# Optimization experiments

Hardware: AMD Instinct MI355X
Metric: run time of the kernel (lower is better)

The kernel has to match this reference:

```python
import jax, jax.numpy as jnp
import numpy as np
import math

B, N, H, TDIM, K, R = 32, 4096, 256, 128, 2, 2


def setup_inputs() -> dict:
    key = jax.random.key(0)
    ks = jax.random.split(key, 12)
    s = 1.0 / math.sqrt(H)
    gain = 1.414
    return {
        "x": jax.random.normal(ks[0], (B, N), jnp.float32),
        "t": jax.random.uniform(ks[1], (B,), jnp.float32),
        # scaled so repeated L@x stays O(1) over Chebyshev hops
        "laplacian": jax.random.normal(ks[2], (N, N), jnp.float32) / math.sqrt(N),
        "w_g1": jax.random.normal(ks[3], (1, H, K + 1), jnp.float32) * gain / math.sqrt(1 + H),
        "w_g2": jax.random.normal(ks[4], (H, 1, K + 1), jnp.float32) * gain / math.sqrt(1 + H),
        "w_t1": jax.random.normal(ks[5], (TDIM, H), jnp.float32) / math.sqrt(TDIM),
        "b_t1": jnp.zeros((H,), jnp.float32),
        "w_t2": jax.random.normal(ks[6], (H, H), jnp.float32) * s,
        "b_t2": jnp.zeros((H,), jnp.float32),
        "w_map": jax.random.normal(ks[7], (N, H), jnp.float32) / math.sqrt(N),
        "b_map": jnp.zeros((H,), jnp.float32),
        "res_w": jax.random.normal(ks[8], (R, 3, H, H), jnp.float32) * s,
        "res_b": jnp.zeros((R, 3, H), jnp.float32),
        "w_o1": jax.random.normal(ks[9], (H, H), jnp.float32) * s,
        "b_o1": jnp.zeros((H,), jnp.float32),
        "w_o2": jax.random.normal(ks[10], (H, N), jnp.float32) * s,
        "b_o2": jnp.zeros((N,), jnp.float32),
    }


def timestep_embedding(t, dim, max_period=10000):
    half = dim // 2  # dim is even here
    freqs = jnp.exp(-math.log(max_period) * jnp.arange(half, dtype=t.dtype) / half)
    args = t[:, None] * freqs[None, :]  # [B, half]
    return jnp.concatenate([jnp.cos(args), jnp.sin(args)], axis=-1)  # [B, dim]


def gcn_layer(L, x, w, conv_order):
    xs = [x]
    h = x
    for _ in range(conv_order):
        h = jnp.einsum('mn,bnc->bmc', L, h)  # sparse-style Laplacian propagation (dense here)
        xs.append(h)
    X = jnp.stack(xs, axis=-1)  # [B, N, C, K+1]
    return jnp.einsum('bnik,iok->bno', X, w)


def reference(x, t, laplacian, w_g1, w_g2, w_t1, b_t1, w_t2, b_t2,
              w_map, b_map, res_w, res_b, w_o1, b_o1, w_o2, b_o2):
    silu = jax.nn.silu
    # time embedding path: sinusoidal -> Linear -> SiLU -> Linear
    temb = timestep_embedding(t, TDIM)
    t_out = silu(temb @ w_t1 + b_t1) @ w_t2 + b_t2  # [B, H]
    # GCNBlock: two Chebyshev GCN layers (GCNLayer.forward applies no activation)
    g = gcn_layer(laplacian, x[:, :, None], w_g1, K)  # [B, N, H]
    g = gcn_layer(laplacian, g, w_g2, K)[..., 0]      # [B, N]
    # ResNet_FC on the node signal
    h = g @ w_map + b_map  # [B, H]
    inv_sqrt2 = 1.0 / math.sqrt(2.0)
    for r in range(R):
        z = h
        for i in range(3):
            z = silu(z @ res_w[r, i] + res_b[r, i])
        h = (h + z) * inv_sqrt2
    # output head with time conditioning
    out = silu((h + t_out) @ w_o1 + b_o1) @ w_o2 + b_o2  # [B, N]
    return out
```

## Files before the change

### kernel.cpp

```cpp
#include <hip/hip_runtime.h>
#include <hip/hip_bf16.h>

typedef __bf16 bf16x8 __attribute__((ext_vector_type(8)));
typedef __bf16 bf16x4 __attribute__((ext_vector_type(4)));
typedef float  f32x4  __attribute__((ext_vector_type(4)));


static constexpr size_t WS_A     = 0;
static constexpr size_t WS_TOUT  = 1024;
static constexpr size_t WS_H0    = 65536;
static constexpr size_t WS_UB    = 131072;
static constexpr size_t WS_XB    = 262144;
static constexpr size_t WS_G2B   = 524288;
static constexpr size_t WS_ZB    = 1048576;
static constexpr size_t WS_ZF    = 2097152;
static constexpr size_t WS_WMAPT = 4194304;
static constexpr size_t WS_WO2T  = 6291456;
static constexpr size_t WS_LB    = 8388608;

__device__ __forceinline__ f32x4 mfma16(bf16x8 a, bf16x8 b, f32x4 c) {
    return __builtin_amdgcn_mfma_f32_16x16x32_bf16(a, b, c, 0, 0, 0);
}

__device__ __forceinline__ bf16x8 cvt8(const float* p) {
    f32x4 lo = *(const f32x4*)p;
    f32x4 hi = *(const f32x4*)(p + 4);
    bf16x8 r;
    r[0] = (__bf16)lo[0]; r[1] = (__bf16)lo[1]; r[2] = (__bf16)lo[2]; r[3] = (__bf16)lo[3];
    r[4] = (__bf16)hi[0]; r[5] = (__bf16)hi[1]; r[6] = (__bf16)hi[2]; r[7] = (__bf16)hi[3];
    return r;
}

__device__ __forceinline__ float silu_f(float x) { return x / (1.0f + __expf(-x)); }

__device__ __forceinline__ void transpose_tile(const float* __restrict__ src, int sstride,
                                               __bf16* __restrict__ dst, int dstride,
                                               int r0, int c0, float* sh, int tid) {
    const int r = tid >> 3, cg = (tid & 7) * 4;
    f32x4 v = *(const f32x4*)(src + (size_t)(r0 + r) * sstride + c0 + cg);
    sh[r * 33 + cg + 0] = v[0];
    sh[r * 33 + cg + 1] = v[1];
    sh[r * 33 + cg + 2] = v[2];
    sh[r * 33 + cg + 3] = v[3];
    __syncthreads();
    bf16x4 o;
    o[0] = (__bf16)sh[(cg + 0) * 33 + r];
    o[1] = (__bf16)sh[(cg + 1) * 33 + r];
    o[2] = (__bf16)sh[(cg + 2) * 33 + r];
    o[3] = (__bf16)sh[(cg + 3) * 33 + r];
    *(bf16x4*)(dst + (size_t)(c0 + r) * dstride + r0 + cg) = o;
}

__global__ __launch_bounds__(256) void prep_kernel(
    const float* __restrict__ x, const float* __restrict__ t,
    const float* __restrict__ w_g1, const float* __restrict__ w_g2,
    const float* __restrict__ w_t1, const float* __restrict__ b_t1,
    const float* __restrict__ w_t2, const float* __restrict__ b_t2,
    const float* __restrict__ w_map, const float* __restrict__ w_o2,
    char* __restrict__ ws)
{
    __shared__ float sh[1056];
    const int bi = blockIdx.x, tid = threadIdx.x;
    if (bi == 0) {
        const float g10 = w_g1[tid * 3 + 0], g11 = w_g1[tid * 3 + 1], g12 = w_g1[tid * 3 + 2];
        const float g20 = w_g2[tid * 3 + 0], g21 = w_g2[tid * 3 + 1], g22 = w_g2[tid * 3 + 2];
        float p[9] = {g10 * g20, g10 * g21, g10 * g22,
                      g11 * g20, g11 * g21, g11 * g22,
                      g12 * g20, g12 * g21, g12 * g22};
        const int wv = tid >> 6, ln = tid & 63;
#pragma unroll
        for (int j = 0; j < 9; ++j) {
            float v = p[j];
#pragma unroll
            for (int off = 32; off > 0; off >>= 1) v += __shfl_down(v, off);
            if (ln == 0) sh[wv * 9 + j] = v;
        }
        __syncthreads();
        if (tid == 0) {
            float s[9];
#pragma unroll
            for (int j = 0; j < 9; ++j) s[j] = sh[j] + sh[9 + j] + sh[18 + j] + sh[27 + j];
            float* a = (float*)(ws + WS_A);
            a[0] = s[0];
            a[1] = s[1] + s[3];
            a[2] = s[2] + s[4] + s[6];
            a[3] = s[5] + s[7];
            a[4] = s[8];
        }
    } else if (bi < 33) {
        const int b = bi - 1;
        float* t_out = (float*)(ws + WS_TOUT);
        if (tid < 64) {
            float fr = __expf(-9.210340371976184f * (float)tid * (1.0f / 64.0f));
            float ang = t[b] * fr;
            sh[tid]      = __cosf(ang);
            sh[64 + tid] = __sinf(ang);
        }
        __syncthreads();
        float acc = b_t1[tid];
        for (int j = 0; j < 128; ++j) acc += sh[j] * w_t1[j * 256 + tid];
        sh[128 + tid] = silu_f(acc);
        __syncthreads();
        float acc2 = b_t2[tid];
        for (int j = 0; j < 256; ++j) acc2 += sh[128 + j] * w_t2[j * 256 + tid];
        t_out[b * 256 + tid] = acc2;
    } else if (bi < 35) {
        f32x4* p = (f32x4*)(ws + WS_H0);
        f32x4 z = {0.f, 0.f, 0.f, 0.f};
        p[(bi - 33) * 256 + tid] = z;
    } else if (bi < 99) {
        const int e = ((bi - 35) * 256 + tid) * 8;
        *(bf16x8*)((__bf16*)(ws + WS_XB) + e) = cvt8(x + e);
    } else if (bi < 1123) {
        const int ti = bi - 99;
        transpose_tile(w_map, 256, (__bf16*)(ws + WS_WMAPT), 4096,
                       (ti >> 3) * 32, (ti & 7) * 32, sh, tid);
    } else {
        const int ti = bi - 1123;
        transpose_tile(w_o2, 4096, (__bf16*)(ws + WS_WO2T), 256,
                       (ti & 7) * 32, (ti >> 3) * 32, sh, tid);
    }
}

__global__ __launch_bounds__(1024) void hop1_kernel(
    const float* __restrict__ L, const __bf16* __restrict__ xb,
    float* __restrict__ zf_out, __bf16* __restrict__ zb_out,
    __bf16* __restrict__ Lb)
{
    __shared__ float red[16][16][33];
    const int bi = blockIdx.x, tid = threadIdx.x;
    const int wave = tid >> 6, lane = tid & 63;
    const int l15 = lane & 15, q = lane >> 4;
    const int m0 = bi * 16;
    const int kbase = wave * 256;

    const float*  lp  = L  + (size_t)(m0 + l15) * 4096;
    __bf16*       lbp = Lb + (size_t)(m0 + l15) * 4096;
    const __bf16* b0p = xb + (size_t)l15 * 4096;
    const __bf16* b1p = xb + (size_t)(l15 + 16) * 4096;

    f32x4 acc0 = {0,0,0,0}, acc1 = {0,0,0,0};
#pragma unroll
    for (int ks = 0; ks < 8; ++ks) {
        const int k = kbase + ks * 32 + q * 8;
        bf16x8 a  = cvt8(lp + k);
        *(bf16x8*)(lbp + k) = a;
        bf16x8 b0 = *(const bf16x8*)(b0p + k);
        bf16x8 b1 = *(const bf16x8*)(b1p + k);
        acc0 = mfma16(a, b0, acc0);
        acc1 = mfma16(a, b1, acc1);
    }
#pragma unroll
    for (int r = 0; r < 4; ++r) {
        red[wave][q * 4 + r][l15]      = acc0[r];
        red[wave][q * 4 + r][l15 + 16] = acc1[r];
    }
    __syncthreads();
    if (tid < 512) {
        const int m = tid & 15, b = tid >> 4;
        float v = 0.f;
#pragma unroll
        for (int w = 0; w < 16; ++w) v += red[w][m][b];
        zf_out[(size_t)b * 4096 + m0 + m] = v;
        zb_out[(size_t)b * 4096 + m0 + m] = (__bf16)v;
    }
}

__global__ __launch_bounds__(1024) void hop_mid_split(
    const __bf16* __restrict__ Lb, const __bf16* __restrict__ zb_in,
    float* __restrict__ zf_out, __bf16* __restrict__ zb_out)
{
    __shared__ float red[16][16][17];
    const int bi = blockIdx.x, tid = threadIdx.x;
    const int wave = tid >> 6, lane = tid & 63;
    const int l15 = lane & 15, q = lane >> 4;
    const int bg = bi & 1;
    const int m0 = (bi >> 1) * 16;
    const int kbase = wave * 256;

    const __bf16* ap  = Lb + (size_t)(m0 + l15) * 4096;
    const __bf16* b0p = zb_in + (size_t)(bg * 16 + l15) * 4096;

    f32x4 acc0 = {0,0,0,0};
#pragma unroll
    for (int ks = 0; ks < 8; ++ks) {
        const int k = kbase + ks * 32 + q * 8;
        bf16x8 a  = *(const bf16x8*)(ap + k);
        bf16x8 b0 = *(const bf16x8*)(b0p + k);
        acc0 = mfma16(a, b0, acc0);
    }
#pragma unroll
    for (int r = 0; r < 4; ++r)
        red[wave][q * 4 + r][l15] = acc0[r];
    __syncthreads();
    if (tid < 256) {
        const int m = tid & 15, b = tid >> 4;
        float v = 0.f;
#pragma unroll
        for (int w = 0; w < 16; ++w) v += red[w][m][b];
        const size_t idx = (size_t)(bg * 16 + b) * 4096 + m0 + m;
        zf_out[idx] = v;
        zb_out[idx] = (__bf16)v;
    }
}

__global__ __launch_bounds__(1024) void hop4_split(
    const __bf16* __restrict__ Lb, const __bf16* __restrict__ zb_in,
    const float* __restrict__ x,
    const float* __restrict__ z1f, const float* __restrict__ z2f,
    const float* __restrict__ z3f, const float* __restrict__ a_c,
    __bf16* __restrict__ g2b)
{
    __shared__ float red[16][16][17];
    const int bi = blockIdx.x, tid = threadIdx.x;
    const int wave = tid >> 6, lane = tid & 63;
    const int l15 = lane & 15, q = lane >> 4;
    const int bg = bi & 1;
    const int m0 = (bi >> 1) * 16;
    const int kbase = wave * 256;

    const __bf16* ap  = Lb + (size_t)(m0 + l15) * 4096;
    const __bf16* b0p = zb_in + (size_t)(bg * 16 + l15) * 4096;

    f32x4 acc0 = {0,0,0,0};
#pragma unroll
    for (int ks = 0; ks < 8; ++ks) {
        const int k = kbase + ks * 32 + q * 8;
        bf16x8 a  = *(const bf16x8*)(ap + k);
        bf16x8 b0 = *(const bf16x8*)(b0p + k);
        acc0 = mfma16(a, b0, acc0);
    }
#pragma unroll
    for (int r = 0; r < 4; ++r)
        red[wave][q * 4 + r][l15] = acc0[r];
    __syncthreads();
    if (tid < 256) {
        const int m = tid & 15, b = tid >> 4;
        float v = 0.f;
#pragma unroll
        for (int w = 0; w < 16; ++w) v += red[w][m][b];
        const size_t idx = (size_t)(bg * 16 + b) * 4096 + m0 + m;
        const float g = a_c[0] * x[idx] + a_c[1] * z1f[idx] + a_c[2] * z2f[idx]
                      + a_c[3] * z3f[idx] + a_c[4] * v;
        g2b[idx] = (__bf16)g;
    }
}

__global__ __launch_bounds__(256) void map_gemm_kernel(
    const __bf16* __restrict__ g2b, const __bf16* __restrict__ w_mapT,
    float* __restrict__ h0)
{
    __shared__ float red[4][16][32];
    const int bi = blockIdx.x, tid = threadIdx.x;
    const int wave = tid >> 6, lane = tid & 63;
    const int l15 = lane & 15, q = lane >> 4;
    const int btile = bi & 1;
    const int hp = (bi >> 1) & 7;
    const int kc = bi >> 4;
    const int kbase = kc * 512 + wave * 128;

    const __bf16* ap  = g2b + (size_t)(btile * 16 + l15) * 4096;
    const __bf16* bp0 = w_mapT + (size_t)(hp * 32 + l15) * 4096;
    const __bf16* bp1 = w_mapT + (size_t)(hp * 32 + 16 + l15) * 4096;

    f32x4 acc0 = {0,0,0,0}, acc1 = {0,0,0,0};
#pragma unroll
    for (int ks = 0; ks < 4; ++ks) {
        const int k = kbase + ks * 32 + q * 8;
        bf16x8 a  = *(const bf16x8*)(ap + k);
        bf16x8 b0 = *(const bf16x8*)(bp0 + k);
        bf16x8 b1 = *(const bf16x8*)(bp1 + k);
        acc0 = mfma16(a, b0, acc0);
        acc1 = mfma16(a, b1, acc1);
    }
#pragma unroll
    for (int r = 0; r < 4; ++r) {
        red[wave][q * 4 + r][l15]      = acc0[r];
        red[wave][q * 4 + r][l15 + 16] = acc1[r];
    }
    __syncthreads();
    const int b_l = tid >> 4, hl = tid & 15;
#pragma unroll
    for (int s = 0; s < 2; ++s) {
        const int h_l = hl + s * 16;
        float v = red[0][b_l][h_l] + red[1][b_l][h_l] + red[2][b_l][h_l] + red[3][b_l][h_l];
        atomicAdd(h0 + (size_t)(btile * 16 + b_l) * 256 + hp * 32 + h_l, v);
    }
}

__global__ __launch_bounds__(1024) void resnet_kernel(
    const float* __restrict__ h0, const float* __restrict__ b_map,
    const float* __restrict__ res_w, const float* __restrict__ res_b,
    const float* __restrict__ t_out, const float* __restrict__ w_o1,
    const float* __restrict__ b_o1, __bf16* __restrict__ u_b)
{
    __shared__ float zs[256];
    __shared__ float part[4][256];
    const int b = blockIdx.x, tid = threadIdx.x;
    const int col = tid & 255, kg = tid >> 8;

    float hv = 0.f;
    if (kg == 0) {
        hv = h0[b * 256 + col] + b_map[col];
        zs[col] = hv;
    }
    __syncthreads();

#pragma unroll
    for (int r = 0; r < 2; ++r) {
        for (int i = 0; i < 3; ++i) {
            const float* W = res_w + ((size_t)(r * 3 + i) << 16) + (size_t)kg * 64 * 256 + col;
            const float* zp = zs + kg * 64;
            float a0 = 0, a1 = 0, a2 = 0, a3 = 0;
#pragma unroll
            for (int j = 0; j < 64; j += 4) {
                a0 += zp[j]     * W[(j)     * 256];
                a1 += zp[j + 1] * W[(j + 1) * 256];
                a2 += zp[j + 2] * W[(j + 2) * 256];
                a3 += zp[j + 3] * W[(j + 3) * 256];
            }
            part[kg][col] = (a0 + a1) + (a2 + a3);
            __syncthreads();
            if (kg == 0) {
                zs[col] = silu_f(res_b[(r * 3 + i) * 256 + col]
                                 + part[0][col] + part[1][col] + part[2][col] + part[3][col]);
            }
            __syncthreads();
        }
        if (kg == 0) {
            hv = (hv + zs[col]) * 0.70710678118654752f;
            zs[col] = hv;
        }
        __syncthreads();
    }

    if (kg == 0) zs[col] = hv + t_out[b * 256 + col];
    __syncthreads();
    {
        const float* W = w_o1 + (size_t)kg * 64 * 256 + col;
        const float* zp = zs + kg * 64;
        float a0 = 0, a1 = 0, a2 = 0, a3 = 0;
#pragma unroll
        for (int j = 0; j < 64; j += 4) {
            a0 += zp[j]     * W[(j)     * 256];
            a1 += zp[j + 1] * W[(j + 1) * 256];
            a2 += zp[j + 2] * W[(j + 2) * 256];
            a3 += zp[j + 3] * W[(j + 3) * 256];
        }
        part[kg][col] = (a0 + a1) + (a2 + a3);
    }
    __syncthreads();
    if (kg == 0) {
        u_b[b * 256 + col] = (__bf16)silu_f(b_o1[col]
            + part[0][col] + part[1][col] + part[2][col] + part[3][col]);
    }
}

__global__ __launch_bounds__(256) void out_gemm_kernel(
    const __bf16* __restrict__ u_b, const __bf16* __restrict__ w_o2T,
    const float* __restrict__ b_o2, float* __restrict__ out)
{
    const int tid = threadIdx.x;
    const int wave = tid >> 6, lane = tid & 63;
    const int l15 = lane & 15, q = lane >> 4;
    const int g = blockIdx.x * 4 + wave;
    const int btile = g & 1;
    const int n0 = (g >> 1) * 32;

    const __bf16* ap  = u_b + (size_t)(btile * 16 + l15) * 256;
    const __bf16* bp0 = w_o2T + (size_t)(n0 + l15) * 256;
    const __bf16* bp1 = w_o2T + (size_t)(n0 + 16 + l15) * 256;

    f32x4 acc0 = {0,0,0,0}, acc1 = {0,0,0,0};
#pragma unroll
    for (int ks = 0; ks < 8; ++ks) {
        const int k = ks * 32 + q * 8;
        bf16x8 a  = *(const bf16x8*)(ap + k);
        bf16x8 b0 = *(const bf16x8*)(bp0 + k);
        bf16x8 b1 = *(const bf16x8*)(bp1 + k);
        acc0 = mfma16(a, b0, acc0);
        acc1 = mfma16(a, b1, acc1);
    }
    const int row = btile * 16 + q * 4;
    const int na = n0 + l15, nb = n0 + 16 + l15;
#pragma unroll
    for (int r = 0; r < 4; ++r) {
        out[(size_t)(row + r) * 4096 + na] = acc0[r] + b_o2[na];
        out[(size_t)(row + r) * 4096 + nb] = acc1[r] + b_o2[nb];
    }
}

extern "C" void kernel_launch(void* const* d_in, const int* in_sizes, int n_in,
                              void* d_out, int out_size, void* d_ws, size_t ws_size,
                              hipStream_t stream)
{
    (void)in_sizes; (void)n_in; (void)out_size; (void)ws_size;
    const float* x     = (const float*)d_in[0];
    const float* t     = (const float*)d_in[1];
    const float* L     = (const float*)d_in[2];
    const float* w_g1  = (const float*)d_in[3];
    const float* w_g2  = (const float*)d_in[4];
    const float* w_t1  = (const float*)d_in[5];
    const float* b_t1  = (const float*)d_in[6];
    const float* w_t2  = (const float*)d_in[7];
    const float* b_t2  = (const float*)d_in[8];
    const float* w_map = (const float*)d_in[9];
    const float* b_map = (const float*)d_in[10];
    const float* res_w = (const float*)d_in[11];
    const float* res_b = (const float*)d_in[12];
    const float* w_o1  = (const float*)d_in[13];
    const float* b_o1  = (const float*)d_in[14];
    const float* w_o2  = (const float*)d_in[15];
    const float* b_o2  = (const float*)d_in[16];
    float* out = (float*)d_out;
    char* ws = (char*)d_ws;

    float*  a_c  = (float*)(ws + WS_A);
    float*  tout = (float*)(ws + WS_TOUT);
    float*  h0   = (float*)(ws + WS_H0);
    __bf16* u_b  = (__bf16*)(ws + WS_UB);
    __bf16* xb   = (__bf16*)(ws + WS_XB);
    __bf16* g2b  = (__bf16*)(ws + WS_G2B);
    __bf16* zb1  = (__bf16*)(ws + WS_ZB);
    __bf16* zb2  = zb1 + 131072;
    __bf16* zb3  = zb2 + 131072;
    float*  z1f  = (float*)(ws + WS_ZF);
    float*  z2f  = z1f + 131072;
    float*  z3f  = z2f + 131072;
    __bf16* w_mapT = (__bf16*)(ws + WS_WMAPT);
    __bf16* w_o2T  = (__bf16*)(ws + WS_WO2T);
    __bf16* Lb     = (__bf16*)(ws + WS_LB);

    prep_kernel<<<2147, 256, 0, stream>>>(x, t, w_g1, w_g2, w_t1, b_t1, w_t2, b_t2,
                                          w_map, w_o2, ws);
    hop1_kernel<<<256, 1024, 0, stream>>>(L, xb, z1f, zb1, Lb);
    hop_mid_split<<<512, 1024, 0, stream>>>(Lb, zb1, z2f, zb2);
    hop_mid_split<<<512, 1024, 0, stream>>>(Lb, zb2, z3f, zb3);
    hop4_split<<<512, 1024, 0, stream>>>(Lb, zb3, x, z1f, z2f, z3f, a_c, g2b);
    map_gemm_kernel<<<128, 256, 0, stream>>>(g2b, w_mapT, h0);
    resnet_kernel<<<32, 1024, 0, stream>>>(h0, b_map, res_w, res_b, tout, w_o1, b_o1, u_b);
    out_gemm_kernel<<<64, 256, 0, stream>>>(u_b, w_o2T, b_o2, out);
}
```

Before: 249.3 us.

## Fuse prep work into first Laplacian hop and merge batch halves in later hops

The separate prep kernel and the first-hop kernel become one 1024-thread launch. Its first 256 blocks do the fp32 L×x hop, converting x to bf16 on the fly instead of going through a staged bf16 copy. The remaining blocks handle the coefficient reduction, time embedding, zeroing and weight transposes, packed four groups per block. The later hop kernels return to one block per 16-row tile covering all 32 batch columns, which halves the grid and reads each L tile once instead of twice. The cost is fewer blocks in flight for the bandwidth-bound hops and heavier fused blocks that use more shared memory.

```diff
diff --git a/kernel.cpp b/kernel.cpp
--- a/kernel.cpp
+++ b/kernel.cpp
@@ -10,7 +10,6 @@
 static constexpr size_t WS_TOUT  = 1024;
 static constexpr size_t WS_H0    = 65536;
 static constexpr size_t WS_UB    = 131072;
-static constexpr size_t WS_XB    = 262144;
 static constexpr size_t WS_G2B   = 524288;
 static constexpr size_t WS_ZB    = 1048576;
 static constexpr size_t WS_ZF    = 2097152;
@@ -33,10 +32,10 @@
 
 __device__ __forceinline__ float silu_f(float x) { return x / (1.0f + __expf(-x)); }
 
-__device__ __forceinline__ void transpose_tile(const float* __restrict__ src, int sstride,
-                                               __bf16* __restrict__ dst, int dstride,
-                                               int r0, int c0, float* sh, int tid) {
-    const int r = tid >> 3, cg = (tid & 7) * 4;
+__device__ __forceinline__ void transpose_tile4(const float* __restrict__ src, int sstride,
+                                                __bf16* __restrict__ dst, int dstride,
+                                                int r0, int c0, float* sh, int stid) {
+    const int r = stid >> 3, cg = (stid & 7) * 4;
     f32x4 v = *(const f32x4*)(src + (size_t)(r0 + r) * sstride + c0 + cg);
     sh[r * 33 + cg + 0] = v[0];
     sh[r * 33 + cg + 1] = v[1];
@@ -51,29 +50,73 @@
     *(bf16x4*)(dst + (size_t)(c0 + r) * dstride + r0 + cg) = o;
 }
 
-__global__ __launch_bounds__(256) void prep_kernel(
-    const float* __restrict__ x, const float* __restrict__ t,
+__global__ __launch_bounds__(1024) void fused1_kernel(
+    const float* __restrict__ L, const float* __restrict__ x,
+    const float* __restrict__ t,
     const float* __restrict__ w_g1, const float* __restrict__ w_g2,
     const float* __restrict__ w_t1, const float* __restrict__ b_t1,
     const float* __restrict__ w_t2, const float* __restrict__ b_t2,
     const float* __restrict__ w_map, const float* __restrict__ w_o2,
     char* __restrict__ ws)
 {
-    __shared__ float sh[1056];
+    __shared__ float sh[8448];
     const int bi = blockIdx.x, tid = threadIdx.x;
-    if (bi == 0) {
-        const float g10 = w_g1[tid * 3 + 0], g11 = w_g1[tid * 3 + 1], g12 = w_g1[tid * 3 + 2];
-        const float g20 = w_g2[tid * 3 + 0], g21 = w_g2[tid * 3 + 1], g22 = w_g2[tid * 3 + 2];
-        float p[9] = {g10 * g20, g10 * g21, g10 * g22,
-                      g11 * g20, g11 * g21, g11 * g22,
-                      g12 * g20, g12 * g21, g12 * g22};
-        const int wv = tid >> 6, ln = tid & 63;
-#pragma unroll
-        for (int j = 0; j < 9; ++j) {
-            float v = p[j];
-#pragma unroll
-            for (int off = 32; off > 0; off >>= 1) v += __shfl_down(v, off);
-            if (ln == 0) sh[wv * 9 + j] = v;
+
+    if (bi < 256) {
+        float*  zf_out = (float*)(ws + WS_ZF);
+        __bf16* zb_out = (__bf16*)(ws + WS_ZB);
+        __bf16* Lb     = (__bf16*)(ws + WS_LB);
+        float (*red)[16][33] = (float(*)[16][33])sh;
+        const int wave = tid >> 6, lane = tid & 63;
+        const int l15 = lane & 15, q = lane >> 4;
+        const int m0 = bi * 16;
+        const int kbase = wave * 256;
+
+        const float* lp  = L  + (size_t)(m0 + l15) * 4096;
+        __bf16*      lbp = Lb + (size_t)(m0 + l15) * 4096;
+        const float* b0p = x + (size_t)l15 * 4096;
+        const float* b1p = x + (size_t)(l15 + 16) * 4096;
+
+        f32x4 acc0 = {0,0,0,0}, acc1 = {0,0,0,0};
+#pragma unroll
+        for (int ks = 0; ks < 8; ++ks) {
+            const int k = kbase + ks * 32 + q * 8;
+            bf16x8 a  = cvt8(lp + k);
+            *(bf16x8*)(lbp + k) = a;
+            bf16x8 b0 = cvt8(b0p + k);
+            bf16x8 b1 = cvt8(b1p + k);
+            acc0 = mfma16(a, b0, acc0);
+            acc1 = mfma16(a, b1, acc1);
+        }
+#pragma unroll
+        for (int r = 0; r < 4; ++r) {
+            red[wave][q * 4 + r][l15]      = acc0[r];
+            red[wave][q * 4 + r][l15 + 16] = acc1[r];
+        }
+        __syncthreads();
+        if (tid < 512) {
+            const int m = tid & 15, b = tid >> 4;
+            float v = 0.f;
+#pragma unroll
+            for (int w = 0; w < 16; ++w) v += red[w][m][b];
+            zf_out[(size_t)b * 4096 + m0 + m] = v;
+            zb_out[(size_t)b * 4096 + m0 + m] = (__bf16)v;
+        }
+    } else if (bi == 256) {
+        if (tid < 256) {
+            const float g10 = w_g1[tid * 3 + 0], g11 = w_g1[tid * 3 + 1], g12 = w_g1[tid * 3 + 2];
+            const float g20 = w_g2[tid * 3 + 0], g21 = w_g2[tid * 3 + 1], g22 = w_g2[tid * 3 + 2];
+            float p[9] = {g10 * g20, g10 * g21, g10 * g22,
+                          g11 * g20, g11 * g21, g11 * g22,
+                          g12 * g20, g12 * g21, g12 * g22};
+            const int wv = tid >> 6, ln = tid & 63;
+#pragma unroll
+            for (int j = 0; j < 9; ++j) {
+                float v = p[j];
+#pragma unroll
+                for (int off = 32; off > 0; off >>= 1) v += __shfl_down(v, off);
+                if (ln == 0) sh[wv * 9 + j] = v;
+            }
         }
         __syncthreads();
         if (tid == 0) {
@@ -87,45 +130,47 @@
             a[3] = s[5] + s[7];
             a[4] = s[8];
         }
-    } else if (bi < 33) {
-        const int b = bi - 1;
+    } else if (bi < 265) {
+        const int grp = tid >> 8, ln = tid & 255;
+        const int b = (bi - 257) * 4 + grp;
+        float* s4 = sh + grp * 384;
         float* t_out = (float*)(ws + WS_TOUT);
-        if (tid < 64) {
-            float fr = __expf(-9.210340371976184f * (float)tid * (1.0f / 64.0f));
+        if (ln < 64) {
+            float fr = __expf(-9.210340371976184f * (float)ln * (1.0f / 64.0f));
             float ang = t[b] * fr;
-            sh[tid]      = __cosf(ang);
-            sh[64 + tid] = __sinf(ang);
+            s4[ln]      = __cosf(ang);
+            s4[64 + ln] = __sinf(ang);
         }
         __syncthreads();
-        float acc = b_t1[tid];
-        for (int j = 0; j < 128; ++j) acc += sh[j] * w_t1[j * 256 + tid];
-        sh[128 + tid] = silu_f(acc);
+        float acc = b_t1[ln];
+        for (int j = 0; j < 128; ++j) acc += s4[j] * w_t1[j * 256 + ln];
+        s4[128 + ln] = silu_f(acc);
         __syncthreads();
-        float acc2 = b_t2[tid];
-        for (int j = 0; j < 256; ++j) acc2 += sh[128 + j] * w_t2[j * 256 + tid];
-        t_out[b * 256 + tid] = acc2;
-    } else if (bi < 35) {
+        float acc2 = b_t2[ln];
+        for (int j = 0; j < 256; ++j) acc2 += s4[128 + j] * w_t2[j * 256 + ln];
+        t_out[b * 256 + ln] = acc2;
+    } else if (bi < 267) {
         f32x4* p = (f32x4*)(ws + WS_H0);
         f32x4 z = {0.f, 0.f, 0.f, 0.f};
-        p[(bi - 33) * 256 + tid] = z;
-    } else if (bi < 99) {
-        const int e = ((bi - 35) * 256 + tid) * 8;
-        *(bf16x8*)((__bf16*)(ws + WS_XB) + e) = cvt8(x + e);
-    } else if (bi < 1123) {
-        const int ti = bi - 99;
-        transpose_tile(w_map, 256, (__bf16*)(ws + WS_WMAPT), 4096,
-                       (ti >> 3) * 32, (ti & 7) * 32, sh, tid);
+        p[(bi - 265) * 1024 + tid] = z;
     } else {
-        const int ti = bi - 1123;
-        transpose_tile(w_o2, 4096, (__bf16*)(ws + WS_WO2T), 256,
-                       (ti & 7) * 32, (ti >> 3) * 32, sh, tid);
-    }
-}
-
-__global__ __launch_bounds__(1024) void hop1_kernel(
-    const float* __restrict__ L, const __bf16* __restrict__ xb,
-    float* __restrict__ zf_out, __bf16* __restrict__ zb_out,
-    __bf16* __restrict__ Lb)
+        const int grp = tid >> 8, stid = tid & 255;
+        const int ti = (bi - 267) * 4 + grp;
+        float* shr = sh + grp * 1080;
+        if (ti < 1024) {
+            transpose_tile4(w_map, 256, (__bf16*)(ws + WS_WMAPT), 4096,
+                            (ti >> 3) * 32, (ti & 7) * 32, shr, stid);
+        } else {
+            const int t2 = ti - 1024;
+            transpose_tile4(w_o2, 4096, (__bf16*)(ws + WS_WO2T), 256,
+                            (t2 & 7) * 32, (t2 >> 3) * 32, shr, stid);
+        }
+    }
+}
+
+__global__ __launch_bounds__(1024) void hop_bf_kernel(
+    const __bf16* __restrict__ Lb, const __bf16* __restrict__ zb_in,
+    float* __restrict__ zf_out, __bf16* __restrict__ zb_out)
 {
     __shared__ float red[16][16][33];
     const int bi = blockIdx.x, tid = threadIdx.x;
@@ -134,17 +179,15 @@
     const int m0 = bi * 16;
     const int kbase = wave * 256;
 
-    const float*  lp  = L  + (size_t)(m0 + l15) * 4096;
-    __bf16*       lbp = Lb + (size_t)(m0 + l15) * 4096;
-    const __bf16* b0p = xb + (size_t)l15 * 4096;
-    const __bf16* b1p = xb + (size_t)(l15 + 16) * 4096;
+    const __bf16* ap  = Lb + (size_t)(m0 + l15) * 4096;
+    const __bf16* b0p = zb_in + (size_t)l15 * 4096;
+    const __bf16* b1p = zb_in + (size_t)(l15 + 16) * 4096;
 
     f32x4 acc0 = {0,0,0,0}, acc1 = {0,0,0,0};
 #pragma unroll
     for (int ks = 0; ks < 8; ++ks) {
         const int k = kbase + ks * 32 + q * 8;
-        bf16x8 a  = cvt8(lp + k);
-        *(bf16x8*)(lbp + k) = a;
+        bf16x8 a  = *(const bf16x8*)(ap + k);
         bf16x8 b0 = *(const bf16x8*)(b0p + k);
         bf16x8 b1 = *(const bf16x8*)(b1p + k);
         acc0 = mfma16(a, b0, acc0);
@@ -166,80 +209,46 @@
     }
 }
 
-__global__ __launch_bounds__(1024) void hop_mid_split(
-    const __bf16* __restrict__ Lb, const __bf16* __restrict__ zb_in,
-    float* __restrict__ zf_out, __bf16* __restrict__ zb_out)
-{
-    __shared__ float red[16][16][17];
-    const int bi = blockIdx.x, tid = threadIdx.x;
-    const int wave = tid >> 6, lane = tid & 63;
-    const int l15 = lane & 15, q = lane >> 4;
-    const int bg = bi & 1;
-    const int m0 = (bi >> 1) * 16;
-    const int kbase = wave * 256;
-
-    const __bf16* ap  = Lb + (size_t)(m0 + l15) * 4096;
-    const __bf16* b0p = zb_in + (size_t)(bg * 16 + l15) * 4096;
-
-    f32x4 acc0 = {0,0,0,0};
-#pragma unroll
-    for (int ks = 0; ks < 8; ++ks) {
-        const int k = kbase + ks * 32 + q * 8;
-        bf16x8 a  = *(const bf16x8*)(ap + k);
-        bf16x8 b0 = *(const bf16x8*)(b0p + k);
-        acc0 = mfma16(a, b0, acc0);
-    }
-#pragma unroll
-    for (int r = 0; r < 4; ++r)
-        red[wave][q * 4 + r][l15] = acc0[r];
-    __syncthreads();
-    if (tid < 256) {
-        const int m = tid & 15, b = tid >> 4;
-        float v = 0.f;
-#pragma unroll
-        for (int w = 0; w < 16; ++w) v += red[w][m][b];
-        const size_t idx = (size_t)(bg * 16 + b) * 4096 + m0 + m;
-        zf_out[idx] = v;
-        zb_out[idx] = (__bf16)v;
-    }
-}
-
-__global__ __launch_bounds__(1024) void hop4_split(
+__global__ __launch_bounds__(1024) void hop4c_kernel(
     const __bf16* __restrict__ Lb, const __bf16* __restrict__ zb_in,
     const float* __restrict__ x,
     const float* __restrict__ z1f, const float* __restrict__ z2f,
     const float* __restrict__ z3f, const float* __restrict__ a_c,
     __bf16* __restrict__ g2b)
 {
-    __shared__ float red[16][16][17];
+    __shared__ float red[16][16][33];
     const int bi = blockIdx.x, tid = threadIdx.x;
     const int wave = tid >> 6, lane = tid & 63;
     const int l15 = lane & 15, q = lane >> 4;
-    const int bg = bi & 1;
-    const int m0 = (bi >> 1) * 16;
+    const int m0 = bi * 16;
     const int kbase = wave * 256;
 
     const __bf16* ap  = Lb + (size_t)(m0 + l15) * 4096;
-    const __bf16* b0p = zb_in + (size_t)(bg * 16 + l15) * 4096;
-
-    f32x4 acc0 = {0,0,0,0};
+    const __bf16* b0p = zb_in + (size_t)l15 * 4096;
+    const __bf16* b1p = zb_in + (size_t)(l15 + 16) * 4096;
+
+    f32x4 acc0 = {0,0,0,0}, acc1 = {0,0,0,0};
 #pragma unroll
     for (int ks = 0; ks < 8; ++ks) {
         const int k = kbase + ks * 32 + q * 8;
         bf16x8 a  = *(const bf16x8*)(ap + k);
         bf16x8 b0 = *(const bf16x8*)(b0p + k);
+        bf16x8 b1 = *(const bf16x8*)(b1p + k);
         acc0 = mfma16(a, b0, acc0);
-    }
-#pragma unroll
-    for (int r = 0; r < 4; ++r)
-        red[wave][q * 4 + r][l15] = acc0[r];
-    __syncthreads();
-    if (tid < 256) {
+        acc1 = mfma16(a, b1, acc1);
+    }
+#pragma unroll
+    for (int r = 0; r < 4; ++r) {
+        red[wave][q * 4 + r][l15]      = acc0[r];
+        red[wave][q * 4 + r][l15 + 16] = acc1[r];
+    }
+    __syncthreads();
+    if (tid < 512) {
         const int m = tid & 15, b = tid >> 4;
         float v = 0.f;
 #pragma unroll
         for (int w = 0; w < 16; ++w) v += red[w][m][b];
-        const size_t idx = (size_t)(bg * 16 + b) * 4096 + m0 + m;
+        const size_t idx = (size_t)b * 4096 + m0 + m;
         const float g = a_c[0] * x[idx] + a_c[1] * z1f[idx] + a_c[2] * z2f[idx]
                       + a_c[3] * z3f[idx] + a_c[4] * v;
         g2b[idx] = (__bf16)g;
@@ -419,7 +428,6 @@
     float*  tout = (float*)(ws + WS_TOUT);
     float*  h0   = (float*)(ws + WS_H0);
     __bf16* u_b  = (__bf16*)(ws + WS_UB);
-    __bf16* xb   = (__bf16*)(ws + WS_XB);
     __bf16* g2b  = (__bf16*)(ws + WS_G2B);
     __bf16* zb1  = (__bf16*)(ws + WS_ZB);
     __bf16* zb2  = zb1 + 131072;
@@ -431,12 +439,11 @@
     __bf16* w_o2T  = (__bf16*)(ws + WS_WO2T);
     __bf16* Lb     = (__bf16*)(ws + WS_LB);
 
-    prep_kernel<<<2147, 256, 0, stream>>>(x, t, w_g1, w_g2, w_t1, b_t1, w_t2, b_t2,
-                                          w_map, w_o2, ws);
-    hop1_kernel<<<256, 1024, 0, stream>>>(L, xb, z1f, zb1, Lb);
-    hop_mid_split<<<512, 1024, 0, stream>>>(Lb, zb1, z2f, zb2);
-    hop_mid_split<<<512, 1024, 0, stream>>>(Lb, zb2, z3f, zb3);
-    hop4_split<<<512, 1024, 0, stream>>>(Lb, zb3, x, z1f, z2f, z3f, a_c, g2b);
+    fused1_kernel<<<779, 1024, 0, stream>>>(L, x, t, w_g1, w_g2, w_t1, b_t1,
+                                            w_t2, b_t2, w_map, w_o2, ws);
+    hop_bf_kernel<<<256, 1024, 0, stream>>>(Lb, zb1, z2f, zb2);
+    hop_bf_kernel<<<256, 1024, 0, stream>>>(Lb, zb2, z3f, zb3);
+    hop4c_kernel<<<256, 1024, 0, stream>>>(Lb, zb3, x, z1f, z2f, z3f, a_c, g2b);
     map_gemm_kernel<<<128, 256, 0, stream>>>(g2b, w_mapT, h0);
     resnet_kernel<<<32, 1024, 0, stream>>>(h0, b_map, res_w, res_b, tout, w_o1, b_o1, u_b);
     out_gemm_kernel<<<64, 256, 0, stream>>>(u_b, w_o2T, b_o2, out);
```

Measured after the change: 246.0 us. Within noise of the previous version (-1.3%).
